# Optimization experiments

Measured on AMD Instinct MI355X. Metric: run time of the kernel, lower is better.

Reference implementation:

```python
import jax, jax.numpy as jnp
import numpy as np

N, E = 50000, 800000
FEAT, NZ, H = 128, 64, 256
IN = FEAT + NZ  # 192
EPS = 1e-5
SLOPE = 0.2


def setup_inputs() -> dict:
    key = jax.random.key(0)
    ks = jax.random.split(key, 16)
    s = 0.02
    return {
        "normal_features": jax.random.normal(ks[0], (N, FEAT), jnp.float32),
        "noise": jax.random.normal(ks[1], (N, NZ), jnp.float32),
        "edge_index": jax.random.randint(ks[2], (2, E), 0, N, jnp.int32),
        "batch": jnp.zeros((N,), jnp.int32),
        # SAGEConv params: lin_l (aggregated neighbors, with bias), lin_r (root, no bias)
        "W_l": jax.random.normal(ks[3], (IN, H), jnp.float32) * s,
        "b_l": jnp.zeros((H,), jnp.float32),
        "W_r": jax.random.normal(ks[4], (IN, H), jnp.float32) * s,
        # BatchNorm (eval mode, running stats)
        "bn_gamma": jnp.ones((H,), jnp.float32),
        "bn_beta": jnp.zeros((H,), jnp.float32),
        "bn_mean": jnp.zeros((H,), jnp.float32),
        "bn_var": jnp.ones((H,), jnp.float32),
        # dense MLP stack
        "fc1_w": jax.random.normal(ks[5], (H, H // 2), jnp.float32) * s,
        "fc1_b": jnp.zeros((H // 2,), jnp.float32),
        "fc2_w": jax.random.normal(ks[6], (H // 2, H // 4), jnp.float32) * s,
        "fc2_b": jnp.zeros((H // 4,), jnp.float32),
        "fc3_w": jax.random.normal(ks[7], (H // 4, H // 4), jnp.float32) * s,
        "fc3_b": jnp.zeros((H // 4,), jnp.float32),
        "fc4_w": jax.random.normal(ks[8], (H // 4, FEAT), jnp.float32) * s,
        "fc4_b": jnp.zeros((FEAT,), jnp.float32),
    }


def _lrelu(x):
    return jnp.where(x >= 0, x, SLOPE * x)


def reference(normal_features, noise, edge_index, batch,
              W_l, b_l, W_r,
              bn_gamma, bn_beta, bn_mean, bn_var,
              fc1_w, fc1_b, fc2_w, fc2_b, fc3_w, fc3_b, fc4_w, fc4_b):
    x = jnp.concatenate([normal_features, noise], axis=1)  # [N, IN]
    src, dst = edge_index[0], edge_index[1]
    # SAGE mean aggregation: gather source features, scatter-add to targets
    msgs = x[src]                                            # [E, IN]
    agg = jax.ops.segment_sum(msgs, dst, num_segments=N)     # [N, IN]
    deg = jax.ops.segment_sum(jnp.ones((E,), x.dtype), dst, num_segments=N)
    mean_agg = agg / jnp.maximum(deg, 1.0)[:, None]
    h = mean_agg @ W_l + b_l + x @ W_r                       # [N, H]
    # BatchNorm (eval) + leaky relu; dropout = identity at inference
    h = (h - bn_mean) * jax.lax.rsqrt(bn_var + EPS) * bn_gamma + bn_beta
    h = _lrelu(h)
    h = _lrelu(h @ fc1_w + fc1_b)
    h = _lrelu(h @ fc2_w + fc2_b)
    h = _lrelu(h @ fc3_w + fc3_b)
    h = _lrelu(h @ fc4_w + fc4_b)                            # [N, FEAT]
    return h
```

## Files before the change

kernel.cpp:

```cpp
#include <hip/hip_runtime.h>

#define N_NODES 50000
#define NPAD    50048
#define FEAT    128
#define NZ      64
#define E_EDGES 800000
#define BN_EPS  1e-5f
#define SLOPE   0.2f
#define NB      196
#define NBUK    391
#define NCHK    128
#define CE      6250

typedef __attribute__((ext_vector_type(8))) short short8v;
typedef __attribute__((ext_vector_type(4))) float f32x4;

__device__ __forceinline__ unsigned short f2bf(float v) {
  union { float f; unsigned u; } c; c.f = v;
  unsigned r = c.u + 0x7FFFu + ((c.u >> 16) & 1u);
  return (unsigned short)(r >> 16);
}
__device__ __forceinline__ float bflo32(unsigned u) {
  union { unsigned x; float f; } c; c.x = u << 16; return c.f;
}
__device__ __forceinline__ float bfhi32(unsigned u) {
  union { unsigned x; float f; } c; c.x = u & 0xFFFF0000u; return c.f;
}

__device__ __forceinline__ void gload16(const void* src, const void* lds) {
  __builtin_amdgcn_global_load_lds(
      (const __attribute__((address_space(1))) unsigned int*)src,
      (__attribute__((address_space(3))) unsigned int*)lds, 16, 0, 0);
}

__global__ __launch_bounds__(256) void xconv_kernel(
    const float* __restrict__ nf, const float* __restrict__ noise,
    unsigned short* __restrict__ xa) {
  int i = blockIdx.x * 256 + threadIdx.x;
  if (i >= N_NODES * 24) return;
  int n = i / 24, s = i % 24;
  float4 va, vb;
  if (s < 16) {
    va = ((const float4*)nf)[(size_t)n * 32 + s * 2];
    vb = ((const float4*)nf)[(size_t)n * 32 + s * 2 + 1];
  } else {
    int t = s - 16;
    va = ((const float4*)noise)[(size_t)n * 16 + t * 2];
    vb = ((const float4*)noise)[(size_t)n * 16 + t * 2 + 1];
  }
  unsigned p0 = (unsigned)f2bf(va.x) | ((unsigned)f2bf(va.y) << 16);
  unsigned p1 = (unsigned)f2bf(va.z) | ((unsigned)f2bf(va.w) << 16);
  unsigned p2 = (unsigned)f2bf(vb.x) | ((unsigned)f2bf(vb.y) << 16);
  unsigned p3 = (unsigned)f2bf(vb.z) | ((unsigned)f2bf(vb.w) << 16);
  *(uint4*)&xa[(size_t)n * 384 + 192 + s * 8] = make_uint4(p0, p1, p2, p3);
}

__global__ __launch_bounds__(256) void hist_kernel(
    const int* __restrict__ ei, int* __restrict__ cnt) {
  __shared__ int h[NBUK];
  int c = blockIdx.x, t = threadIdx.x;
  for (int i = t; i < NBUK; i += 256) h[i] = 0;
  __syncthreads();
  int e0 = c * CE;
  for (int e = e0 + t; e < e0 + CE; e += 256)
    atomicAdd(&h[ei[E_EDGES + e] >> 7], 1);
  __syncthreads();
  for (int i = t; i < NBUK; i += 256) cnt[i * NCHK + c] = h[i];
}

template <int LEN>
__global__ __launch_bounds__(256) void block_sum_kernel(
    const int* __restrict__ in, int* __restrict__ bsum) {
  __shared__ int sh[256];
  int i = blockIdx.x * 256 + threadIdx.x;
  sh[threadIdx.x] = (i < LEN) ? in[i] : 0;
  __syncthreads();
  for (int s = 128; s > 0; s >>= 1) {
    if (threadIdx.x < s) sh[threadIdx.x] += sh[threadIdx.x + s];
    __syncthreads();
  }
  if (threadIdx.x == 0) bsum[blockIdx.x] = sh[0];
}

__global__ __launch_bounds__(256) void scan_bsum_kernel(int* __restrict__ bsum) {
  __shared__ int sh[256];
  int t = threadIdx.x;
  sh[t] = (t < NB) ? bsum[t] : 0;
  __syncthreads();
  for (int off = 1; off < 256; off <<= 1) {
    int v = (t >= off) ? sh[t - off] : 0;
    __syncthreads();
    sh[t] += v;
    __syncthreads();
  }
  if (t < NB) bsum[t] = (t == 0) ? 0 : sh[t - 1];
}

template <int LEN>
__global__ __launch_bounds__(256) void scan_chunk_kernel(
    const int* __restrict__ in, const int* __restrict__ bsum,
    int* __restrict__ out) {
  __shared__ int sh[256];
  int t = threadIdx.x;
  int i = blockIdx.x * 256 + t;
  int v = (i < LEN) ? in[i] : 0;
  sh[t] = v;
  __syncthreads();
  for (int off = 1; off < 256; off <<= 1) {
    int u = (t >= off) ? sh[t - off] : 0;
    __syncthreads();
    sh[t] += u;
    __syncthreads();
  }
  if (i < LEN) out[i] = bsum[blockIdx.x] + sh[t] - v;
}

__global__ __launch_bounds__(256) void scatter_kernel(
    const int* __restrict__ ei, const int* __restrict__ ebase,
    unsigned* __restrict__ ebuf) {
  __shared__ int cur[NBUK];
  int c = blockIdx.x, t = threadIdx.x;
  for (int i = t; i < NBUK; i += 256) cur[i] = ebase[i * NCHK + c];
  __syncthreads();
  int e0 = c * CE;
  for (int e = e0 + t; e < e0 + CE; e += 256) {
    int s = ei[e], d = ei[E_EDGES + e];
    int p = atomicAdd(&cur[d >> 7], 1);
    ebuf[p] = ((unsigned)(d & 127) << 16) | (unsigned)s;
  }
}

__global__ __launch_bounds__(256) void sortb_kernel(
    const unsigned* __restrict__ ebuf, const int* __restrict__ ebase,
    int* __restrict__ csr, int* __restrict__ deg, int* __restrict__ cursor) {
  __shared__ int h[128], sc[128], curn[128];
  int b = blockIdx.x, t = threadIdx.x;
  int beg = ebase[b * NCHK];
  int endb = (b == NBUK - 1) ? E_EDGES : ebase[(b + 1) * NCHK];
  if (t < 128) h[t] = 0;
  __syncthreads();
  for (int i = beg + t; i < endb; i += 256) atomicAdd(&h[ebuf[i] >> 16], 1);
  __syncthreads();
  if (t < 128) sc[t] = h[t];
  __syncthreads();
  for (int off = 1; off < 128; off <<= 1) {
    int v = (t >= off && t < 128) ? sc[t - off] : 0;
    __syncthreads();
    if (t < 128) sc[t] += v;
    __syncthreads();
  }
  if (t < 128) {
    curn[t] = sc[t] - h[t];
    int n = b * 128 + t;
    if (n < N_NODES) {
      deg[n] = h[t];
      cursor[n] = beg + sc[t];
    }
  }
  __syncthreads();
  for (int i = beg + t; i < endb; i += 256) {
    unsigned u = ebuf[i];
    int p = atomicAdd(&curn[u >> 16], 1);
    csr[beg + p] = (int)(u & 0xFFFFu) * 768 + 384;
  }
}

__global__ __launch_bounds__(256) void gather_kernel(
    const int* __restrict__ csr, const int* __restrict__ cursor,
    const int* __restrict__ deg, unsigned short* __restrict__ xa) {
  int wid = (blockIdx.x * blockDim.x + threadIdx.x) >> 6;
  int lane = threadIdx.x & 63;
  if (wid >= N_NODES) return;
  int d = deg[wid];
  int end = cursor[wid];
  int start = end - d;
  const bool act = lane < 48;
  const char* base = (const char*)xa + (size_t)(lane * 8);

  float a0 = 0.f, a1 = 0.f, a2 = 0.f, a3 = 0.f;
  float b0 = 0.f, b1 = 0.f, b2 = 0.f, b3 = 0.f;
  int j = start;
  for (; j + 7 < end; j += 8) {
    int o0 = csr[j],     o1 = csr[j + 1], o2 = csr[j + 2], o3 = csr[j + 3];
    int o4 = csr[j + 4], o5 = csr[j + 5], o6 = csr[j + 6], o7 = csr[j + 7];
    if (act) {
      uint2 v0 = *(const uint2*)(base + o0);
      uint2 v1 = *(const uint2*)(base + o1);
      uint2 v2 = *(const uint2*)(base + o2);
      uint2 v3 = *(const uint2*)(base + o3);
      uint2 v4 = *(const uint2*)(base + o4);
      uint2 v5 = *(const uint2*)(base + o5);
      uint2 v6 = *(const uint2*)(base + o6);
      uint2 v7 = *(const uint2*)(base + o7);
      a0 += bflo32(v0.x) + bflo32(v2.x) + bflo32(v4.x) + bflo32(v6.x);
      a1 += bfhi32(v0.x) + bfhi32(v2.x) + bfhi32(v4.x) + bfhi32(v6.x);
      a2 += bflo32(v0.y) + bflo32(v2.y) + bflo32(v4.y) + bflo32(v6.y);
      a3 += bfhi32(v0.y) + bfhi32(v2.y) + bfhi32(v4.y) + bfhi32(v6.y);
      b0 += bflo32(v1.x) + bflo32(v3.x) + bflo32(v5.x) + bflo32(v7.x);
      b1 += bfhi32(v1.x) + bfhi32(v3.x) + bfhi32(v5.x) + bfhi32(v7.x);
      b2 += bflo32(v1.y) + bflo32(v3.y) + bflo32(v5.y) + bflo32(v7.y);
      b3 += bfhi32(v1.y) + bfhi32(v3.y) + bfhi32(v5.y) + bfhi32(v7.y);
    }
  }
  for (; j < end; ++j) {
    int o = csr[j];
    if (act) {
      uint2 v = *(const uint2*)(base + o);
      a0 += bflo32(v.x); a1 += bfhi32(v.x);
      a2 += bflo32(v.y); a3 += bfhi32(v.y);
    }
  }
  if (act) {
    float inv = 1.0f / fmaxf((float)d, 1.0f);
    float m0 = (a0 + b0) * inv, m1 = (a1 + b1) * inv;
    float m2 = (a2 + b2) * inv, m3 = (a3 + b3) * inv;
    unsigned r0 = (unsigned)f2bf(m0) | ((unsigned)f2bf(m1) << 16);
    unsigned r1 = (unsigned)f2bf(m2) | ((unsigned)f2bf(m3) << 16);
    *(uint2*)&xa[(size_t)wid * 384 + (size_t)lane * 4] = make_uint2(r0, r1);
  }
}

__global__ __launch_bounds__(256) void wconv_kernel(
    const float* __restrict__ Wl, const float* __restrict__ Wr,
    const float* __restrict__ W1, const float* __restrict__ W2,
    const float* __restrict__ W3, const float* __restrict__ W4,
    unsigned short* __restrict__ Wc_, unsigned short* __restrict__ W1_,
    unsigned short* __restrict__ W2_, unsigned short* __restrict__ W3_,
    unsigned short* __restrict__ W4_) {
  int idx = blockIdx.x * 256 + threadIdx.x;
  if (idx < 49152) {
    int k = idx % 192, m = idx / 192;
    Wc_[(size_t)m * 384 + k] = f2bf(Wl[(size_t)k * 256 + m]);
  } else if (idx < 98304) {
    int local = idx - 49152;
    int k = local % 192, m = local / 192;
    Wc_[(size_t)m * 384 + 192 + k] = f2bf(Wr[(size_t)k * 256 + m]);
  } else if (idx < 131072) {
    int local = idx - 98304;
    int k = local % 256, m = local / 256;
    W1_[(size_t)m * 256 + k] = f2bf(W1[(size_t)k * 128 + m]);
  } else if (idx < 139264) {
    int local = idx - 131072;
    int k = local % 128, m = local / 128;
    W2_[(size_t)m * 128 + k] = f2bf(W2[(size_t)k * 64 + m]);
  } else if (idx < 143360) {
    int local = idx - 139264;
    int k = local % 64, m = local / 64;
    W3_[(size_t)m * 64 + k] = f2bf(W3[(size_t)k * 64 + m]);
  } else if (idx < 151552) {
    int local = idx - 143360;
    int k = local % 64, m = local / 64;
    W4_[(size_t)m * 64 + k] = f2bf(W4[(size_t)k * 128 + m]);
  }
}

template <int KBASE, int ALD, int OUTLD, int OUT_MODE, bool PAIR>
__global__ __launch_bounds__(256) void gemm_plain(
    const unsigned short* __restrict__ Ab, const unsigned short* __restrict__ Bb,
    const float* __restrict__ bias, const float* __restrict__ gamma,
    const float* __restrict__ beta, const float* __restrict__ bmean,
    const float* __restrict__ bvar, unsigned short* __restrict__ outp) {
  constexpr int BM = 128, BK = 64;
  constexpr int NITER = KBASE / BK;
  constexpr int GRB = NPAD / 128;

  __shared__ unsigned short lds[16384];
  unsigned short* sA = lds;
  unsigned short* sB = lds + 8192;

  const int tid = threadIdx.x;
  const int wid = tid >> 6;
  const int lane = tid & 63;

  int rb, cb;
  if (PAIR) {
    int bid = blockIdx.x;
    int g = bid >> 4, r = bid & 15;
    int rem = GRB - g * 8; if (rem > 8) rem = 8;
    cb = (r >= rem) ? 1 : 0;
    rb = g * 8 + (cb ? r - rem : r);
  } else {
    rb = blockIdx.x; cb = 0;
  }
  const int rowbase = rb * BM;
  const int colbase = cb * 128;
  const int wr = wid >> 1, wc = wid & 1;

  f32x4 acc[4][4];
#pragma unroll
  for (int i = 0; i < 4; ++i)
#pragma unroll
    for (int j = 0; j < 4; ++j) acc[i][j] = (f32x4)0.f;

  for (int kt = 0; kt < NITER; ++kt) {
    const int kb = kt * BK;
    __syncthreads();
#pragma unroll
    for (int j = 0; j < 4; ++j) {
      int o = j * 4 + wid;
      int row = o * 8 + (lane >> 3);
      int slog = (lane & 7) ^ (lane >> 3);
      const char* src = (const char*)Bb +
          ((size_t)(colbase + row) * KBASE + kb) * 2 + (size_t)slog * 16;
      gload16(src, sB + o * 512);
    }
#pragma unroll
    for (int j = 0; j < 4; ++j) {
      int o = j * 4 + wid;
      int row = o * 8 + (lane >> 3);
      int slog = (lane & 7) ^ (lane >> 3);
      const char* src = (const char*)Ab +
          ((size_t)(rowbase + row) * ALD + kb) * 2 + (size_t)slog * 16;
      gload16(src, sA + o * 512);
    }
    __syncthreads();

#pragma unroll
    for (int kk = 0; kk < 2; ++kk) {
      short8v a[4], b[4];
#pragma unroll
      for (int fi = 0; fi < 4; ++fi) {
        int rt = wr * 64 + fi * 16 + (lane & 15);
        int sl = (kk * 4 + (lane >> 4)) ^ (rt & 7);
        a[fi] = *(const short8v*)&sA[rt * 64 + sl * 8];
      }
#pragma unroll
      for (int fj = 0; fj < 4; ++fj) {
        int ct = wc * 64 + fj * 16 + (lane & 15);
        int sl = (kk * 4 + (lane >> 4)) ^ (ct & 7);
        b[fj] = *(const short8v*)&sB[ct * 64 + sl * 8];
      }
#pragma unroll
      for (int fi = 0; fi < 4; ++fi)
#pragma unroll
        for (int fj = 0; fj < 4; ++fj)
          acc[fi][fj] = __builtin_amdgcn_mfma_f32_16x16x32_bf16(
              a[fi], b[fj], acc[fi][fj], 0, 0, 0);
    }
  }

  __syncthreads();
#pragma unroll
  for (int fj = 0; fj < 4; ++fj) {
    int gcl = wc * 64 + fj * 16 + (lane & 15);
    int gc = colbase + gcl;
    float sc, sh;
    if (OUT_MODE == 0) {
      float s = gamma[gc] * rsqrtf(bvar[gc] + BN_EPS);
      sc = s; sh = bias[gc] * s + beta[gc] - bmean[gc] * s;
    } else {
      sc = 1.f; sh = bias[gc];
    }
#pragma unroll
    for (int fi = 0; fi < 4; ++fi)
#pragma unroll
      for (int r = 0; r < 4; ++r) {
        int rt = wr * 64 + fi * 16 + ((lane >> 4) << 2) + r;
        float v = acc[fi][fj][r] * sc + sh;
        v = (v >= 0.f) ? v : SLOPE * v;
        lds[rt * 128 + gcl] = f2bf(v);
      }
  }
  __syncthreads();
#pragma unroll
  for (int i0 = 0; i0 < 8; ++i0) {
    int i = tid + i0 * 256;
    int row = i >> 4, u4 = i & 15;
    ((uint4*)(outp + (size_t)(rowbase + row) * OUTLD + colbase))[u4] =
        ((const uint4*)lds)[i];
  }
}

__global__ __launch_bounds__(256) void fc234_kernel(
    const unsigned short* __restrict__ h1p,
    const unsigned short* __restrict__ W2_, const unsigned short* __restrict__ W3_,
    const unsigned short* __restrict__ W4_,
    const float* __restrict__ b2, const float* __restrict__ b3,
    const float* __restrict__ b4, float* __restrict__ outp) {
  __shared__ unsigned short lds[32768];
  unsigned short* SA  = lds;
  unsigned short* SB  = lds + 16384;
  unsigned short* SH2 = lds + 24576;

  const int tid = threadIdx.x;
  const int wid = tid >> 6;
  const int lane = tid & 63;
  const int rowbase = blockIdx.x * 128;
  const int wr = wid >> 1, wc = wid & 1;

#pragma unroll
  for (int j = 0; j < 8; ++j) {
    int o = j * 4 + wid;
    int rloc = o * 4 + (lane >> 4);
    int slog = (lane & 15) ^ ((rloc & 7) << 1);
    const char* src = (const char*)h1p +
        ((size_t)(rowbase + rloc) * 128) * 2 + (size_t)slog * 16;
    gload16(src, SA + o * 512);
  }
#pragma unroll
  for (int j = 0; j < 4; ++j) {
    int o = j * 4 + wid;
    int rloc = o * 4 + (lane >> 4);
    int slog = (lane & 15) ^ ((rloc & 7) << 1);
    const char* src = (const char*)W2_ +
        ((size_t)rloc * 128) * 2 + (size_t)slog * 16;
    gload16(src, SB + o * 512);
  }
  __syncthreads();

  f32x4 acc2[4][2];
#pragma unroll
  for (int i = 0; i < 4; ++i) { acc2[i][0] = (f32x4)0.f; acc2[i][1] = (f32x4)0.f; }
#pragma unroll
  for (int kk = 0; kk < 4; ++kk) {
    short8v a[4], b[2];
#pragma unroll
    for (int fi = 0; fi < 4; ++fi) {
      int rt = wr * 64 + fi * 16 + (lane & 15);
      int ph = (kk * 4 + (lane >> 4)) ^ ((rt & 7) << 1);
      a[fi] = *(const short8v*)&SA[rt * 128 + ph * 8];
    }
#pragma unroll
    for (int fj = 0; fj < 2; ++fj) {
      int ct = wc * 32 + fj * 16 + (lane & 15);
      int ph = (kk * 4 + (lane >> 4)) ^ ((ct & 7) << 1);
      b[fj] = *(const short8v*)&SB[ct * 128 + ph * 8];
    }
#pragma unroll
    for (int fi = 0; fi < 4; ++fi)
#pragma unroll
      for (int fj = 0; fj < 2; ++fj)
        acc2[fi][fj] = __builtin_amdgcn_mfma_f32_16x16x32_bf16(
            a[fi], b[fj], acc2[fi][fj], 0, 0, 0);
  }
  __syncthreads();

#pragma unroll
  for (int fj = 0; fj < 2; ++fj) {
    int gc = wc * 32 + fj * 16 + (lane & 15);
    float bb = b2[gc];
#pragma unroll
    for (int fi = 0; fi < 4; ++fi)
#pragma unroll
      for (int r = 0; r < 4; ++r) {
        int rt = wr * 64 + fi * 16 + ((lane >> 4) << 2) + r;
        float v = acc2[fi][fj][r] + bb;
        v = (v >= 0.f) ? v : SLOPE * v;
        SH2[rt * 64 + ((gc >> 3) ^ (rt & 7)) * 8 + (gc & 7)] = f2bf(v);
      }
  }
#pragma unroll
  for (int j = 0; j < 2; ++j) {
    int o = j * 4 + wid;
    int rloc = o * 8 + (lane >> 3);
    int slog = (lane & 7) ^ (lane >> 3);
    const char* src = (const char*)W3_ +
        ((size_t)rloc * 64) * 2 + (size_t)slog * 16;
    gload16(src, SB + o * 512);
  }
  __syncthreads();

  f32x4 acc3[4][2];
#pragma unroll
  for (int i = 0; i < 4; ++i) { acc3[i][0] = (f32x4)0.f; acc3[i][1] = (f32x4)0.f; }
#pragma unroll
  for (int kk = 0; kk < 2; ++kk) {
    short8v a[4], b[2];
#pragma unroll
    for (int fi = 0; fi < 4; ++fi) {
      int rt = wr * 64 + fi * 16 + (lane & 15);
      int ph = (kk * 4 + (lane >> 4)) ^ (rt & 7);
      a[fi] = *(const short8v*)&SH2[rt * 64 + ph * 8];
    }
#pragma unroll
    for (int fj = 0; fj < 2; ++fj) {
      int ct = wc * 32 + fj * 16 + (lane & 15);
      int ph = (kk * 4 + (lane >> 4)) ^ (ct & 7);
      b[fj] = *(const short8v*)&SB[ct * 64 + ph * 8];
    }
#pragma unroll
    for (int fi = 0; fi < 4; ++fi)
#pragma unroll
      for (int fj = 0; fj < 2; ++fj)
        acc3[fi][fj] = __builtin_amdgcn_mfma_f32_16x16x32_bf16(
            a[fi], b[fj], acc3[fi][fj], 0, 0, 0);
  }
  __syncthreads();

  unsigned short* SH3 = SA;
#pragma unroll
  for (int fj = 0; fj < 2; ++fj) {
    int gc = wc * 32 + fj * 16 + (lane & 15);
    float bb = b3[gc];
#pragma unroll
    for (int fi = 0; fi < 4; ++fi)
#pragma unroll
      for (int r = 0; r < 4; ++r) {
        int rt = wr * 64 + fi * 16 + ((lane >> 4) << 2) + r;
        float v = acc3[fi][fj][r] + bb;
        v = (v >= 0.f) ? v : SLOPE * v;
        SH3[rt * 64 + ((gc >> 3) ^ (rt & 7)) * 8 + (gc & 7)] = f2bf(v);
      }
  }
#pragma unroll
  for (int j = 0; j < 4; ++j) {
    int o = j * 4 + wid;
    int rloc = o * 8 + (lane >> 3);
    int slog = (lane & 7) ^ (lane >> 3);
    const char* src = (const char*)W4_ +
        ((size_t)rloc * 64) * 2 + (size_t)slog * 16;
    gload16(src, SB + o * 512);
  }
  __syncthreads();

  f32x4 acc4[4][4];
#pragma unroll
  for (int i = 0; i < 4; ++i)
#pragma unroll
    for (int j = 0; j < 4; ++j) acc4[i][j] = (f32x4)0.f;
#pragma unroll
  for (int kk = 0; kk < 2; ++kk) {
    short8v a[4], b[4];
#pragma unroll
    for (int fi = 0; fi < 4; ++fi) {
      int rt = wr * 64 + fi * 16 + (lane & 15);
      int ph = (kk * 4 + (lane >> 4)) ^ (rt & 7);
      a[fi] = *(const short8v*)&SH3[rt * 64 + ph * 8];
    }
#pragma unroll
    for (int fj = 0; fj < 4; ++fj) {
      int ct = wc * 64 + fj * 16 + (lane & 15);
      int ph = (kk * 4 + (lane >> 4)) ^ (ct & 7);
      b[fj] = *(const short8v*)&SB[ct * 64 + ph * 8];
    }
#pragma unroll
    for (int fi = 0; fi < 4; ++fi)
#pragma unroll
      for (int fj = 0; fj < 4; ++fj)
        acc4[fi][fj] = __builtin_amdgcn_mfma_f32_16x16x32_bf16(
            a[fi], b[fj], acc4[fi][fj], 0, 0, 0);
  }

  const int crow0 = rowbase + wr * 64;
#pragma unroll
  for (int fj = 0; fj < 4; ++fj) {
    int gc = wc * 64 + fj * 16 + (lane & 15);
    float bb = b4[gc];
#pragma unroll
    for (int fi = 0; fi < 4; ++fi)
#pragma unroll
      for (int r = 0; r < 4; ++r) {
        int gr = crow0 + fi * 16 + ((lane >> 4) << 2) + r;
        if (gr < N_NODES) {
          float v = acc4[fi][fj][r] + bb;
          v = (v >= 0.f) ? v : SLOPE * v;
          outp[(size_t)gr * FEAT + gc] = v;
        }
      }
  }
}

extern "C" void kernel_launch(void* const* d_in, const int* in_sizes, int n_in,
                              void* d_out, int out_size, void* d_ws, size_t ws_size,
                              hipStream_t stream) {
  const float* nf    = (const float*)d_in[0];
  const float* noise = (const float*)d_in[1];
  const int*   ei    = (const int*)d_in[2];
  const float* Wl    = (const float*)d_in[4];
  const float* bl    = (const float*)d_in[5];
  const float* Wr    = (const float*)d_in[6];
  const float* gam   = (const float*)d_in[7];
  const float* bet   = (const float*)d_in[8];
  const float* bmean = (const float*)d_in[9];
  const float* bvar  = (const float*)d_in[10];
  const float* fc1w  = (const float*)d_in[11];
  const float* fc1b  = (const float*)d_in[12];
  const float* fc2w  = (const float*)d_in[13];
  const float* fc2b  = (const float*)d_in[14];
  const float* fc3w  = (const float*)d_in[15];
  const float* fc3b  = (const float*)d_in[16];
  const float* fc4w  = (const float*)d_in[17];
  const float* fc4b  = (const float*)d_in[18];
  float* outp = (float*)d_out;

  unsigned short* xa  = (unsigned short*)d_ws;
  unsigned short* hp  = xa + (size_t)NPAD * 384;
  unsigned short* Wc_ = hp + (size_t)NPAD * 256;
  unsigned short* W1_ = Wc_ + 256 * 384;
  unsigned short* W2_ = W1_ + 128 * 256;
  unsigned short* W3_ = W2_ + 64 * 128;
  unsigned short* W4_ = W3_ + 64 * 64;
  int* deg    = (int*)(W4_ + 128 * 64);
  int* cursor = deg + N_NODES;
  int* bsum   = cursor + N_NODES;
  int* cnt    = bsum + 256;
  int* ebase  = cnt + NBUK * NCHK;
  unsigned short* h1p = xa;
  int*      csr  = (int*)d_out;
  unsigned* ebuf = (unsigned*)d_out + E_EDGES;

  wconv_kernel<<<592, 256, 0, stream>>>(Wl, Wr, fc1w, fc2w, fc3w, fc4w,
                                        Wc_, W1_, W2_, W3_, W4_);
  xconv_kernel<<<(N_NODES * 24 + 255) / 256, 256, 0, stream>>>(nf, noise, xa);

  hist_kernel<<<NCHK, 256, 0, stream>>>(ei, cnt);
  block_sum_kernel<NBUK * NCHK><<<NB, 256, 0, stream>>>(cnt, bsum);
  scan_bsum_kernel<<<1, 256, 0, stream>>>(bsum);
  scan_chunk_kernel<NBUK * NCHK><<<NB, 256, 0, stream>>>(cnt, bsum, ebase);
  scatter_kernel<<<NCHK, 256, 0, stream>>>(ei, ebase, ebuf);
  sortb_kernel<<<NBUK, 256, 0, stream>>>(ebuf, ebase, csr, deg, cursor);

  gather_kernel<<<(N_NODES + 3) / 4, 256, 0, stream>>>(csr, cursor, deg, xa);

  const int RB = NPAD / 128;

  gemm_plain<384, 384, 256, 0, true><<<2 * RB, 256, 0, stream>>>(
      xa, Wc_, bl, gam, bet, bmean, bvar, hp);
  gemm_plain<256, 256, 128, 1, false><<<RB, 256, 0, stream>>>(
      hp, W1_, fc1b, nullptr, nullptr, nullptr, nullptr, h1p);
  fc234_kernel<<<RB, 256, 0, stream>>>(h1p, W2_, W3_, W4_,
                                       fc2b, fc3b, fc4b, outp);
}
```

Before: 151.7 us.

## Fuse SAGE GEMM and full MLP chain into one kernel; merge prep kernels

Merges weight conversion, feature conversion and edge histogram into a single prep launch. It replaces the two GEMM kernels and the fc2-4 kernel with one gemm_chain kernel, so the 256-wide hidden activations and fc1 output stay in LDS instead of round-tripping through global memory. The trade-offs are much larger LDS use per block (80KB) and more accumulator registers (4x8 tiles), which cuts occupancy. Each block now also computes all 256 output columns, so the grid drops to 391 blocks.

After: 161.8 us. 1.07x slower.

```diff
diff --git a/kernel.cpp b/kernel.cpp
--- a/kernel.cpp
+++ b/kernel.cpp
@@ -11,6 +11,7 @@
 #define NBUK    391
 #define NCHK    128
 #define CE      6250
+#define XCONV_B 4688
 
 typedef __attribute__((ext_vector_type(8))) short short8v;
 typedef __attribute__((ext_vector_type(4))) float f32x4;
@@ -26,46 +27,82 @@
 __device__ __forceinline__ float bfhi32(unsigned u) {
   union { unsigned x; float f; } c; c.x = u & 0xFFFF0000u; return c.f;
 }
-
 __device__ __forceinline__ void gload16(const void* src, const void* lds) {
   __builtin_amdgcn_global_load_lds(
       (const __attribute__((address_space(1))) unsigned int*)src,
       (__attribute__((address_space(3))) unsigned int*)lds, 16, 0, 0);
 }
-
-__global__ __launch_bounds__(256) void xconv_kernel(
+__device__ __forceinline__ float lrelu(float v) {
+  return (v >= 0.f) ? v : SLOPE * v;
+}
+
+__global__ __launch_bounds__(256) void prep_kernel(
     const float* __restrict__ nf, const float* __restrict__ noise,
-    unsigned short* __restrict__ xa) {
-  int i = blockIdx.x * 256 + threadIdx.x;
-  if (i >= N_NODES * 24) return;
-  int n = i / 24, s = i % 24;
-  float4 va, vb;
-  if (s < 16) {
-    va = ((const float4*)nf)[(size_t)n * 32 + s * 2];
-    vb = ((const float4*)nf)[(size_t)n * 32 + s * 2 + 1];
+    const int* __restrict__ ei,
+    const float* __restrict__ Wl, const float* __restrict__ Wr,
+    const float* __restrict__ W1, const float* __restrict__ W2,
+    const float* __restrict__ W3, const float* __restrict__ W4,
+    unsigned short* __restrict__ xa,
+    unsigned short* __restrict__ Wc_, unsigned short* __restrict__ W1_,
+    unsigned short* __restrict__ W2_, unsigned short* __restrict__ W3_,
+    unsigned short* __restrict__ W4_, int* __restrict__ cnt) {
+  __shared__ int h[NBUK];
+  int b = blockIdx.x, t = threadIdx.x;
+  if (b < 592) {
+    int idx = b * 256 + t;
+    if (idx < 49152) {
+      int k = idx % 192, m = idx / 192;
+      Wc_[(size_t)m * 384 + k] = f2bf(Wl[(size_t)k * 256 + m]);
+    } else if (idx < 98304) {
+      int local = idx - 49152;
+      int k = local % 192, m = local / 192;
+      Wc_[(size_t)m * 384 + 192 + k] = f2bf(Wr[(size_t)k * 256 + m]);
+    } else if (idx < 131072) {
+      int local = idx - 98304;
+      int k = local % 256, m = local / 256;
+      W1_[(size_t)m * 256 + k] = f2bf(W1[(size_t)k * 128 + m]);
+    } else if (idx < 139264) {
+      int local = idx - 131072;
+      int k = local % 128, m = local / 128;
+      W2_[(size_t)m * 128 + k] = f2bf(W2[(size_t)k * 64 + m]);
+    } else if (idx < 143360) {
+      int local = idx - 139264;
+      int k = local % 64, m = local / 64;
+      W3_[(size_t)m * 64 + k] = f2bf(W3[(size_t)k * 64 + m]);
+    } else if (idx < 151552) {
+      int local = idx - 143360;
+      int k = local % 64, m = local / 64;
+      W4_[(size_t)m * 64 + k] = f2bf(W4[(size_t)k * 128 + m]);
+    }
+  } else if (b < 592 + XCONV_B) {
+    int i = (b - 592) * 256 + t;
+    if (i < N_NODES * 24) {
+      int n = i / 24, s = i % 24;
+      float4 va, vb;
+      if (s < 16) {
+        va = ((const float4*)nf)[(size_t)n * 32 + s * 2];
+        vb = ((const float4*)nf)[(size_t)n * 32 + s * 2 + 1];
+      } else {
+        int u = s - 16;
+        va = ((const float4*)noise)[(size_t)n * 16 + u * 2];
+        vb = ((const float4*)noise)[(size_t)n * 16 + u * 2 + 1];
+      }
+      unsigned p0 = (unsigned)f2bf(va.x) | ((unsigned)f2bf(va.y) << 16);
+      unsigned p1 = (unsigned)f2bf(va.z) | ((unsigned)f2bf(va.w) << 16);
+      unsigned p2 = (unsigned)f2bf(vb.x) | ((unsigned)f2bf(vb.y) << 16);
+      unsigned p3 = (unsigned)f2bf(vb.z) | ((unsigned)f2bf(vb.w) << 16);
+      *(uint4*)&xa[(size_t)n * 384 + 192 + s * 8] = make_uint4(p0, p1, p2, p3);
+    }
   } else {
-    int t = s - 16;
-    va = ((const float4*)noise)[(size_t)n * 16 + t * 2];
-    vb = ((const float4*)noise)[(size_t)n * 16 + t * 2 + 1];
-  }
-  unsigned p0 = (unsigned)f2bf(va.x) | ((unsigned)f2bf(va.y) << 16);
-  unsigned p1 = (unsigned)f2bf(va.z) | ((unsigned)f2bf(va.w) << 16);
-  unsigned p2 = (unsigned)f2bf(vb.x) | ((unsigned)f2bf(vb.y) << 16);
-  unsigned p3 = (unsigned)f2bf(vb.z) | ((unsigned)f2bf(vb.w) << 16);
-  *(uint4*)&xa[(size_t)n * 384 + 192 + s * 8] = make_uint4(p0, p1, p2, p3);
-}
-
-__global__ __launch_bounds__(256) void hist_kernel(
-    const int* __restrict__ ei, int* __restrict__ cnt) {
-  __shared__ int h[NBUK];
-  int c = blockIdx.x, t = threadIdx.x;
-  for (int i = t; i < NBUK; i += 256) h[i] = 0;
-  __syncthreads();
-  int e0 = c * CE;
-  for (int e = e0 + t; e < e0 + CE; e += 256)
-    atomicAdd(&h[ei[E_EDGES + e] >> 7], 1);
-  __syncthreads();
-  for (int i = t; i < NBUK; i += 256) cnt[i * NCHK + c] = h[i];
+    int c = b - (592 + XCONV_B);
+    for (int i = t; i < NBUK; i += 256) h[i] = 0;
+    __syncthreads();
+    int e0 = c * CE;
+    for (int e = e0 + t; e < e0 + CE; e += 256)
+      atomicAdd(&h[ei[E_EDGES + e] >> 7], 1);
+    __syncthreads();
+    for (int i = t; i < NBUK; i += 256) cnt[i * NCHK + c] = h[i];
+  }
 }
 
 template <int LEN>
@@ -220,191 +257,173 @@
   }
 }
 
-__global__ __launch_bounds__(256) void wconv_kernel(
-    const float* __restrict__ Wl, const float* __restrict__ Wr,
-    const float* __restrict__ W1, const float* __restrict__ W2,
-    const float* __restrict__ W3, const float* __restrict__ W4,
-    unsigned short* __restrict__ Wc_, unsigned short* __restrict__ W1_,
-    unsigned short* __restrict__ W2_, unsigned short* __restrict__ W3_,
-    unsigned short* __restrict__ W4_) {
-  int idx = blockIdx.x * 256 + threadIdx.x;
-  if (idx < 49152) {
-    int k = idx % 192, m = idx / 192;
-    Wc_[(size_t)m * 384 + k] = f2bf(Wl[(size_t)k * 256 + m]);
-  } else if (idx < 98304) {
-    int local = idx - 49152;
-    int k = local % 192, m = local / 192;
-    Wc_[(size_t)m * 384 + 192 + k] = f2bf(Wr[(size_t)k * 256 + m]);
-  } else if (idx < 131072) {
-    int local = idx - 98304;
-    int k = local % 256, m = local / 256;
-    W1_[(size_t)m * 256 + k] = f2bf(W1[(size_t)k * 128 + m]);
-  } else if (idx < 139264) {
-    int local = idx - 131072;
-    int k = local % 128, m = local / 128;
-    W2_[(size_t)m * 128 + k] = f2bf(W2[(size_t)k * 64 + m]);
-  } else if (idx < 143360) {
-    int local = idx - 139264;
-    int k = local % 64, m = local / 64;
-    W3_[(size_t)m * 64 + k] = f2bf(W3[(size_t)k * 64 + m]);
-  } else if (idx < 151552) {
-    int local = idx - 143360;
-    int k = local % 64, m = local / 64;
-    W4_[(size_t)m * 64 + k] = f2bf(W4[(size_t)k * 128 + m]);
-  }
-}
-
-template <int KBASE, int ALD, int OUTLD, int OUT_MODE, bool PAIR>
-__global__ __launch_bounds__(256) void gemm_plain(
-    const unsigned short* __restrict__ Ab, const unsigned short* __restrict__ Bb,
-    const float* __restrict__ bias, const float* __restrict__ gamma,
-    const float* __restrict__ beta, const float* __restrict__ bmean,
-    const float* __restrict__ bvar, unsigned short* __restrict__ outp) {
-  constexpr int BM = 128, BK = 64;
-  constexpr int NITER = KBASE / BK;
-  constexpr int GRB = NPAD / 128;
-
-  __shared__ unsigned short lds[16384];
-  unsigned short* sA = lds;
-  unsigned short* sB = lds + 8192;
+__global__ __launch_bounds__(256) void gemm_chain(
+    const unsigned short* __restrict__ xa, const unsigned short* __restrict__ Wc_,
+    const unsigned short* __restrict__ W1_, const unsigned short* __restrict__ W2_,
+    const unsigned short* __restrict__ W3_, const unsigned short* __restrict__ W4_,
+    const float* __restrict__ bl, const float* __restrict__ gam,
+    const float* __restrict__ bet, const float* __restrict__ bmean,
+    const float* __restrict__ bvar, const float* __restrict__ b1,
+    const float* __restrict__ b2, const float* __restrict__ b3,
+    const float* __restrict__ b4, float* __restrict__ outp) {
+  __shared__ unsigned short lds[40960];
+  unsigned short* X = lds;
+  unsigned short* Y = lds + 32768;
 
   const int tid = threadIdx.x;
   const int wid = tid >> 6;
   const int lane = tid & 63;
-
-  int rb, cb;
-  if (PAIR) {
-    int bid = blockIdx.x;
-    int g = bid >> 4, r = bid & 15;
-    int rem = GRB - g * 8; if (rem > 8) rem = 8;
-    cb = (r >= rem) ? 1 : 0;
-    rb = g * 8 + (cb ? r - rem : r);
-  } else {
-    rb = blockIdx.x; cb = 0;
-  }
-  const int rowbase = rb * BM;
-  const int colbase = cb * 128;
+  const int g = lane >> 4;
+  const int rowbase = blockIdx.x * 128;
   const int wr = wid >> 1, wc = wid & 1;
-
-  f32x4 acc[4][4];
+  const int slog = (lane & 7) ^ (lane >> 3);
+
+  f32x4 acc[4][8];
 #pragma unroll
   for (int i = 0; i < 4; ++i)
 #pragma unroll
-    for (int j = 0; j < 4; ++j) acc[i][j] = (f32x4)0.f;
-
-  for (int kt = 0; kt < NITER; ++kt) {
-    const int kb = kt * BK;
-    __syncthreads();
+    for (int j = 0; j < 8; ++j) acc[i][j] = (f32x4)0.f;
+
+  for (int kt = 0; kt < 6; ++kt) {
+    const int kb = kt * 64;
+    __syncthreads();
+#pragma unroll
+    for (int j = 0; j < 8; ++j) {
+      int o = j * 4 + wid;
+      int row = o * 8 + (lane >> 3);
+      gload16((const char*)Wc_ + ((size_t)row * 384 + kb) * 2 + (size_t)slog * 16,
+              X + 8192 + o * 512);
+    }
 #pragma unroll
     for (int j = 0; j < 4; ++j) {
       int o = j * 4 + wid;
       int row = o * 8 + (lane >> 3);
-      int slog = (lane & 7) ^ (lane >> 3);
-      const char* src = (const char*)Bb +
-          ((size_t)(colbase + row) * KBASE + kb) * 2 + (size_t)slog * 16;
-      gload16(src, sB + o * 512);
-    }
-#pragma unroll
-    for (int j = 0; j < 4; ++j) {
-      int o = j * 4 + wid;
-      int row = o * 8 + (lane >> 3);
-      int slog = (lane & 7) ^ (lane >> 3);
-      const char* src = (const char*)Ab +
-          ((size_t)(rowbase + row) * ALD + kb) * 2 + (size_t)slog * 16;
-      gload16(src, sA + o * 512);
-    }
-    __syncthreads();
-
+      gload16((const char*)xa + ((size_t)(rowbase + row) * 384 + kb) * 2 +
+                  (size_t)slog * 16,
+              X + o * 512);
+    }
+    __syncthreads();
+
+#pragma unroll
+    for (int kk = 0; kk < 2; ++kk) {
+      short8v a[4];
+#pragma unroll
+      for (int fi = 0; fi < 4; ++fi) {
+        int rt = wr * 64 + fi * 16 + (lane & 15);
+        int sl = (kk * 4 + g) ^ (rt & 7);
+        a[fi] = *(const short8v*)&X[rt * 64 + sl * 8];
+      }
+#pragma unroll
+      for (int fjh = 0; fjh < 2; ++fjh) {
+        short8v b[4];
+#pragma unroll
+        for (int q = 0; q < 4; ++q) {
+          int ct = wc * 128 + (fjh * 4 + q) * 16 + (lane & 15);
+          int sl = (kk * 4 + g) ^ (ct & 7);
+          b[q] = *(const short8v*)&X[8192 + ct * 64 + sl * 8];
+        }
+#pragma unroll
+        for (int fi = 0; fi < 4; ++fi)
+#pragma unroll
+          for (int q = 0; q < 4; ++q)
+            acc[fi][fjh * 4 + q] = __builtin_amdgcn_mfma_f32_16x16x32_bf16(
+                a[fi], b[q], acc[fi][fjh * 4 + q], 0, 0, 0);
+      }
+    }
+  }
+
+  __syncthreads();
+#pragma unroll
+  for (int fj = 0; fj < 8; ++fj) {
+    int gc = wc * 128 + fj * 16 + (lane & 15);
+    float s = gam[gc] * rsqrtf(bvar[gc] + BN_EPS);
+    float sh = bl[gc] * s + bet[gc] - bmean[gc] * s;
+    int lc = gc & 127;
+#pragma unroll
+    for (int fi = 0; fi < 4; ++fi)
+#pragma unroll
+      for (int r = 0; r < 4; ++r) {
+        int rt = wr * 64 + fi * 16 + (g << 2) + r;
+        float v = lrelu(acc[fi][fj][r] * s + sh);
+        X[wc * 16384 + rt * 128 + (((lc >> 3) ^ ((rt & 7) << 1)) << 3) +
+          (lc & 7)] = f2bf(v);
+      }
+  }
+#pragma unroll
+  for (int j = 0; j < 4; ++j) {
+    int o = j * 4 + wid;
+    int col = o * 8 + (lane >> 3);
+    gload16((const char*)W1_ + ((size_t)col * 256) * 2 + (size_t)slog * 16,
+            Y + o * 512);
+  }
+  __syncthreads();
+
+  f32x4 acc1[4][4];
+#pragma unroll
+  for (int i = 0; i < 4; ++i)
+#pragma unroll
+    for (int j = 0; j < 4; ++j) acc1[i][j] = (f32x4)0.f;
+
+  for (int kt = 0; kt < 4; ++kt) {
+    if (kt) {
+      __syncthreads();
+#pragma unroll
+      for (int j = 0; j < 4; ++j) {
+        int o = j * 4 + wid;
+        int col = o * 8 + (lane >> 3);
+        gload16((const char*)W1_ + ((size_t)col * 256 + kt * 64) * 2 +
+                    (size_t)slog * 16,
+                Y + o * 512);
+      }
+      __syncthreads();
+    }
+    const int half = kt >> 1;
+    const int lkb8 = (kt & 1) * 8;
 #pragma unroll
     for (int kk = 0; kk < 2; ++kk) {
       short8v a[4], b[4];
 #pragma unroll
       for (int fi = 0; fi < 4; ++fi) {
         int rt = wr * 64 + fi * 16 + (lane & 15);
-        int sl = (kk * 4 + (lane >> 4)) ^ (rt & 7);
-        a[fi] = *(const short8v*)&sA[rt * 64 + sl * 8];
+        int ph = (lkb8 + kk * 4 + g) ^ ((rt & 7) << 1);
+        a[fi] = *(const short8v*)&X[half * 16384 + rt * 128 + ph * 8];
       }
 #pragma unroll
       for (int fj = 0; fj < 4; ++fj) {
         int ct = wc * 64 + fj * 16 + (lane & 15);
-        int sl = (kk * 4 + (lane >> 4)) ^ (ct & 7);
-        b[fj] = *(const short8v*)&sB[ct * 64 + sl * 8];
+        int sl = (kk * 4 + g) ^ (ct & 7);
+        b[fj] = *(const short8v*)&Y[ct * 64 + sl * 8];
       }
 #pragma unroll
       for (int fi = 0; fi < 4; ++fi)
 #pragma unroll
         for (int fj = 0; fj < 4; ++fj)
-          acc[fi][fj] = __builtin_amdgcn_mfma_f32_16x16x32_bf16(
-              a[fi], b[fj], acc[fi][fj], 0, 0, 0);
+          acc1[fi][fj] = __builtin_amdgcn_mfma_f32_16x16x32_bf16(
+              a[fi], b[fj], acc1[fi][fj], 0, 0, 0);
     }
   }
 
   __syncthreads();
 #pragma unroll
   for (int fj = 0; fj < 4; ++fj) {
-    int gcl = wc * 64 + fj * 16 + (lane & 15);
-    int gc = colbase + gcl;
-    float sc, sh;
-    if (OUT_MODE == 0) {
-      float s = gamma[gc] * rsqrtf(bvar[gc] + BN_EPS);
-      sc = s; sh = bias[gc] * s + beta[gc] - bmean[gc] * s;
-    } else {
-      sc = 1.f; sh = bias[gc];
-    }
+    int gc = wc * 64 + fj * 16 + (lane & 15);
+    float bb = b1[gc];
 #pragma unroll
     for (int fi = 0; fi < 4; ++fi)
 #pragma unroll
       for (int r = 0; r < 4; ++r) {
-        int rt = wr * 64 + fi * 16 + ((lane >> 4) << 2) + r;
-        float v = acc[fi][fj][r] * sc + sh;
-        v = (v >= 0.f) ? v : SLOPE * v;
-        lds[rt * 128 + gcl] = f2bf(v);
-      }
-  }
-  __syncthreads();
-#pragma unroll
-  for (int i0 = 0; i0 < 8; ++i0) {
-    int i = tid + i0 * 256;
-    int row = i >> 4, u4 = i & 15;
-    ((uint4*)(outp + (size_t)(rowbase + row) * OUTLD + colbase))[u4] =
-        ((const uint4*)lds)[i];
-  }
-}
-
-__global__ __launch_bounds__(256) void fc234_kernel(
-    const unsigned short* __restrict__ h1p,
-    const unsigned short* __restrict__ W2_, const unsigned short* __restrict__ W3_,
-    const unsigned short* __restrict__ W4_,
-    const float* __restrict__ b2, const float* __restrict__ b3,
-    const float* __restrict__ b4, float* __restrict__ outp) {
-  __shared__ unsigned short lds[32768];
-  unsigned short* SA  = lds;
-  unsigned short* SB  = lds + 16384;
-  unsigned short* SH2 = lds + 24576;
-
-  const int tid = threadIdx.x;
-  const int wid = tid >> 6;
-  const int lane = tid & 63;
-  const int rowbase = blockIdx.x * 128;
-  const int wr = wid >> 1, wc = wid & 1;
-
-#pragma unroll
-  for (int j = 0; j < 8; ++j) {
-    int o = j * 4 + wid;
-    int rloc = o * 4 + (lane >> 4);
-    int slog = (lane & 15) ^ ((rloc & 7) << 1);
-    const char* src = (const char*)h1p +
-        ((size_t)(rowbase + rloc) * 128) * 2 + (size_t)slog * 16;
-    gload16(src, SA + o * 512);
+        int rt = wr * 64 + fi * 16 + (g << 2) + r;
+        float v = lrelu(acc1[fi][fj][r] + bb);
+        X[rt * 128 + (((gc >> 3) ^ ((rt & 7) << 1)) << 3) + (gc & 7)] = f2bf(v);
+      }
   }
 #pragma unroll
   for (int j = 0; j < 4; ++j) {
     int o = j * 4 + wid;
     int rloc = o * 4 + (lane >> 4);
-    int slog = (lane & 15) ^ ((rloc & 7) << 1);
-    const char* src = (const char*)W2_ +
-        ((size_t)rloc * 128) * 2 + (size_t)slog * 16;
-    gload16(src, SB + o * 512);
+    int sl4 = (lane & 15) ^ ((rloc & 7) << 1);
+    gload16((const char*)W2_ + ((size_t)rloc * 128) * 2 + (size_t)sl4 * 16,
+            Y + o * 512);
   }
   __syncthreads();
 
@@ -417,14 +436,14 @@
 #pragma unroll
     for (int fi = 0; fi < 4; ++fi) {
       int rt = wr * 64 + fi * 16 + (lane & 15);
-      int ph = (kk * 4 + (lane >> 4)) ^ ((rt & 7) << 1);
-      a[fi] = *(const short8v*)&SA[rt * 128 + ph * 8];
+      int ph = (kk * 4 + g) ^ ((rt & 7) << 1);
+      a[fi] = *(const short8v*)&X[rt * 128 + ph * 8];
     }
 #pragma unroll
     for (int fj = 0; fj < 2; ++fj) {
       int ct = wc * 32 + fj * 16 + (lane & 15);
-      int ph = (kk * 4 + (lane >> 4)) ^ ((ct & 7) << 1);
-      b[fj] = *(const short8v*)&SB[ct * 128 + ph * 8];
+      int ph = (kk * 4 + g) ^ ((ct & 7) << 1);
+      b[fj] = *(const short8v*)&Y[ct * 128 + ph * 8];
     }
 #pragma unroll
     for (int fi = 0; fi < 4; ++fi)
@@ -433,8 +452,8 @@
         acc2[fi][fj] = __builtin_amdgcn_mfma_f32_16x16x32_bf16(
             a[fi], b[fj], acc2[fi][fj], 0, 0, 0);
   }
-  __syncthreads();
-
+
+  __syncthreads();
 #pragma unroll
   for (int fj = 0; fj < 2; ++fj) {
     int gc = wc * 32 + fj * 16 + (lane & 15);
@@ -443,20 +462,17 @@
     for (int fi = 0; fi < 4; ++fi)
 #pragma unroll
       for (int r = 0; r < 4; ++r) {
-        int rt = wr * 64 + fi * 16 + ((lane >> 4) << 2) + r;
-        float v = acc2[fi][fj][r] + bb;
-        v = (v >= 0.f) ? v : SLOPE * v;
-        SH2[rt * 64 + ((gc >> 3) ^ (rt & 7)) * 8 + (gc & 7)] = f2bf(v);
+        int rt = wr * 64 + fi * 16 + (g << 2) + r;
+        float v = lrelu(acc2[fi][fj][r] + bb);
+        X[16384 + rt * 64 + (((gc >> 3) ^ (rt & 7)) << 3) + (gc & 7)] = f2bf(v);
       }
   }
 #pragma unroll
   for (int j = 0; j < 2; ++j) {
     int o = j * 4 + wid;
     int rloc = o * 8 + (lane >> 3);
-    int slog = (lane & 7) ^ (lane >> 3);
-    const char* src = (const char*)W3_ +
-        ((size_t)rloc * 64) * 2 + (size_t)slog * 16;
-    gload16(src, SB + o * 512);
+    gload16((const char*)W3_ + ((size_t)rloc * 64) * 2 + (size_t)slog * 16,
+            Y + o * 512);
   }
   __syncthreads();
 
@@ -469,14 +485,14 @@
 #pragma unroll
     for (int fi = 0; fi < 4; ++fi) {
       int rt = wr * 64 + fi * 16 + (lane & 15);
-      int ph = (kk * 4 + (lane >> 4)) ^ (rt & 7);
-      a[fi] = *(const short8v*)&SH2[rt * 64 + ph * 8];
+      int sl = (kk * 4 + g) ^ (rt & 7);
+      a[fi] = *(const short8v*)&X[16384 + rt * 64 + sl * 8];
     }
 #pragma unroll
     for (int fj = 0; fj < 2; ++fj) {
       int ct = wc * 32 + fj * 16 + (lane & 15);
-      int ph = (kk * 4 + (lane >> 4)) ^ (ct & 7);
-      b[fj] = *(const short8v*)&SB[ct * 64 + ph * 8];
+      int sl = (kk * 4 + g) ^ (ct & 7);
+      b[fj] = *(const short8v*)&Y[ct * 64 + sl * 8];
     }
 #pragma unroll
     for (int fi = 0; fi < 4; ++fi)
@@ -485,9 +501,8 @@
         acc3[fi][fj] = __builtin_amdgcn_mfma_f32_16x16x32_bf16(
             a[fi], b[fj], acc3[fi][fj], 0, 0, 0);
   }
-  __syncthreads();
-
-  unsigned short* SH3 = SA;
+
+  __syncthreads();
 #pragma unroll
   for (int fj = 0; fj < 2; ++fj) {
     int gc = wc * 32 + fj * 16 + (lane & 15);
@@ -496,20 +511,17 @@
     for (int fi = 0; fi < 4; ++fi)
 #pragma unroll
       for (int r = 0; r < 4; ++r) {
-        int rt = wr * 64 + fi * 16 + ((lane >> 4) << 2) + r;
-        float v = acc3[fi][fj][r] + bb;
-        v = (v >= 0.f) ? v : SLOPE * v;
-        SH3[rt * 64 + ((gc >> 3) ^ (rt & 7)) * 8 + (gc & 7)] = f2bf(v);
+        int rt = wr * 64 + fi * 16 + (g << 2) + r;
+        float v = lrelu(acc3[fi][fj][r] + bb);
+        X[24576 + rt * 64 + (((gc >> 3) ^ (rt & 7)) << 3) + (gc & 7)] = f2bf(v);
       }
   }
 #pragma unroll
   for (int j = 0; j < 4; ++j) {
     int o = j * 4 + wid;
     int rloc = o * 8 + (lane >> 3);
-    int slog = (lane & 7) ^ (lane >> 3);
-    const char* src = (const char*)W4_ +
-        ((size_t)rloc * 64) * 2 + (size_t)slog * 16;
-    gload16(src, SB + o * 512);
+    gload16((const char*)W4_ + ((size_t)rloc * 64) * 2 + (size_t)slog * 16,
+            Y + o * 512);
   }
   __syncthreads();
 
@@ -524,14 +536,14 @@
 #pragma unroll
     for (int fi = 0; fi < 4; ++fi) {
       int rt = wr * 64 + fi * 16 + (lane & 15);
-      int ph = (kk * 4 + (lane >> 4)) ^ (rt & 7);
-      a[fi] = *(const short8v*)&SH3[rt * 64 + ph * 8];
+      int sl = (kk * 4 + g) ^ (rt & 7);
+      a[fi] = *(const short8v*)&X[24576 + rt * 64 + sl * 8];
     }
 #pragma unroll
     for (int fj = 0; fj < 4; ++fj) {
       int ct = wc * 64 + fj * 16 + (lane & 15);
-      int ph = (kk * 4 + (lane >> 4)) ^ (ct & 7);
-      b[fj] = *(const short8v*)&SB[ct * 64 + ph * 8];
+      int sl = (kk * 4 + g) ^ (ct & 7);
+      b[fj] = *(const short8v*)&Y[ct * 64 + sl * 8];
     }
 #pragma unroll
     for (int fi = 0; fi < 4; ++fi)
@@ -550,10 +562,9 @@
     for (int fi = 0; fi < 4; ++fi)
 #pragma unroll
       for (int r = 0; r < 4; ++r) {
-        int gr = crow0 + fi * 16 + ((lane >> 4) << 2) + r;
+        int gr = crow0 + fi * 16 + (g << 2) + r;
         if (gr < N_NODES) {
-          float v = acc4[fi][fj][r] + bb;
-          v = (v >= 0.f) ? v : SLOPE * v;
+          float v = lrelu(acc4[fi][fj][r] + bb);
           outp[(size_t)gr * FEAT + gc] = v;
         }
       }
@@ -584,8 +595,7 @@
   float* outp = (float*)d_out;
 
   unsigned short* xa  = (unsigned short*)d_ws;
-  unsigned short* hp  = xa + (size_t)NPAD * 384;
-  unsigned short* Wc_ = hp + (size_t)NPAD * 256;
+  unsigned short* Wc_ = xa + (size_t)NPAD * 384;
   unsigned short* W1_ = Wc_ + 256 * 384;
   unsigned short* W2_ = W1_ + 128 * 256;
   unsigned short* W3_ = W2_ + 64 * 128;
@@ -595,15 +605,13 @@
   int* bsum   = cursor + N_NODES;
   int* cnt    = bsum + 256;
   int* ebase  = cnt + NBUK * NCHK;
-  unsigned short* h1p = xa;
   int*      csr  = (int*)d_out;
   unsigned* ebuf = (unsigned*)d_out + E_EDGES;
 
-  wconv_kernel<<<592, 256, 0, stream>>>(Wl, Wr, fc1w, fc2w, fc3w, fc4w,
-                                        Wc_, W1_, W2_, W3_, W4_);
-  xconv_kernel<<<(N_NODES * 24 + 255) / 256, 256, 0, stream>>>(nf, noise, xa);
-
-  hist_kernel<<<NCHK, 256, 0, stream>>>(ei, cnt);
+  prep_kernel<<<592 + XCONV_B + NCHK, 256, 0, stream>>>(
+      nf, noise, ei, Wl, Wr, fc1w, fc2w, fc3w, fc4w,
+      xa, Wc_, W1_, W2_, W3_, W4_, cnt);
+
   block_sum_kernel<NBUK * NCHK><<<NB, 256, 0, stream>>>(cnt, bsum);
   scan_bsum_kernel<<<1, 256, 0, stream>>>(bsum);
   scan_chunk_kernel<NBUK * NCHK><<<NB, 256, 0, stream>>>(cnt, bsum, ebase);
@@ -612,12 +620,7 @@
 
   gather_kernel<<<(N_NODES + 3) / 4, 256, 0, stream>>>(csr, cursor, deg, xa);
 
-  const int RB = NPAD / 128;
-
-  gemm_plain<384, 384, 256, 0, true><<<2 * RB, 256, 0, stream>>>(
-      xa, Wc_, bl, gam, bet, bmean, bvar, hp);
-  gemm_plain<256, 256, 128, 1, false><<<RB, 256, 0, stream>>>(
-      hp, W1_, fc1b, nullptr, nullptr, nullptr, nullptr, h1p);
-  fc234_kernel<<<RB, 256, 0, stream>>>(h1p, W2_, W3_, W4_,
-                                       fc2b, fc3b, fc4b, outp);
-}
+  gemm_chain<<<NPAD / 128, 256, 0, stream>>>(
+      xa, Wc_, W1_, W2_, W3_, W4_,
+      bl, gam, bet, bmean, bvar, fc1b, fc2b, fc3b, fc4b, outp);
+}
```
